# Kernel tuning notes

Measured on AMD Instinct MI355X. Metric: run time of the kernel, lower is better.

The kernel has to match this reference:

```python
import jax, jax.numpy as jnp
from jax import lax
import numpy as np


def setup_inputs() -> dict:
    key = jax.random.key(0)
    ks = jax.random.split(key, 10)
    B, C, T, H, W = 4, 128, 32, 24, 24
    M, k_t, k_s, mix_k = 3, 3, 3, 3
    s = 0.05
    q = jax.random.normal(ks[0], (B, C, T, H, W), jnp.float32)
    k = jax.random.normal(ks[1], (B, C, T, H, W), jnp.float32)
    v = jax.random.normal(ks[2], (B, C, T, H, W), jnp.float32)
    # depthwise 3D kernel banks: [M, C, 1, k_t, k_s, k_s] (OIDHW per branch, groups=C)
    Wk = jax.random.normal(ks[3], (M, C, 1, k_t, k_s, k_s), jnp.float32) * s
    Wv = jax.random.normal(ks[4], (M, C, 1, k_t, k_s, k_s), jnp.float32) * s
    # mix predictor: 1x1 conv1d (pointwise) + causal conv1d C->M
    pre_w = jax.random.normal(ks[5], (C, C), jnp.float32) * s
    pre_b = jax.random.normal(ks[6], (C,), jnp.float32) * s
    mix_w = jax.random.normal(ks[7], (M, C, mix_k), jnp.float32) * s
    mix_b = jax.random.normal(ks[8], (M,), jnp.float32) * s
    return {"q": q, "k": k, "v": v, "Wk": Wk, "Wv": Wv,
            "pre_w": pre_w, "pre_b": pre_b, "mix_w": mix_w, "mix_b": mix_b}


def _mix_alpha(q, pre_w, pre_b, mix_w, mix_b):
    # q: [B,C,T,H,W] -> global spatial pool -> [B,C,T]
    qg = q.mean(axis=(3, 4))
    h = jnp.einsum('oc,bct->bot', pre_w, qg) + pre_b[None, :, None]
    h = jax.nn.gelu(h, approximate=False)  # torch nn.GELU default = exact
    mix_k = mix_w.shape[-1]
    logits = lax.conv_general_dilated(
        h, mix_w, window_strides=(1,), padding=[(mix_k - 1, 0)],
        dimension_numbers=('NCH', 'OIH', 'NCH')) + mix_b[None, :, None]
    return jax.nn.softmax(logits, axis=1)  # [B,M,T]


def _dwconv3d_causal(x, w):
    # x: [B,C,T,H,W], w: [C,1,k_t,k_h,k_w] depthwise (groups=C)
    C = x.shape[1]
    k_t, k_h, k_w = w.shape[2], w.shape[3], w.shape[4]
    pad = [(k_t - 1, 0), (k_h // 2, k_h // 2), (k_w // 2, k_w // 2)]
    return lax.conv_general_dilated(
        x, w, window_strides=(1, 1, 1), padding=pad,
        dimension_numbers=('NCDHW', 'OIDHW', 'NCDHW'),
        feature_group_count=C)


def reference(q, k, v, Wk, Wv, pre_w, pre_b, mix_w, mix_b):
    alpha = _mix_alpha(q, pre_w, pre_b, mix_w, mix_b)  # [B,M,T]
    # all M depthwise branches at once: [M,B,C,T,H,W]
    km = jax.vmap(_dwconv3d_causal, in_axes=(None, 0))(k, Wk)
    vm = jax.vmap(_dwconv3d_causal, in_axes=(None, 0))(v, Wv)
    # per-time mixture-weighted sum over M
    k_out = jnp.einsum('mbcthw,bmt->bcthw', km, alpha)
    v_out = jnp.einsum('mbcthw,bmt->bcthw', vm, alpha)
    return (k_out, v_out)
```

## Files before the change

### kernel.cpp

```cpp
#include <hip/hip_runtime.h>
#include <math.h>

namespace {
constexpr int Bn = 4, Cn = 128, Tn = 32, Hn = 24, Wn = 24, Mn = 3;
constexpr int HWn = Hn * Wn;
constexpr int TTile = 8;
constexpr int PL = TTile + 2;
constexpr int RS = 28;
constexpr int PSr = 26 * RS;
}

__global__ __launch_bounds__(256) void pool_kernel(const float* __restrict__ q,
                                                   float* __restrict__ qg) {
    int wave = threadIdx.x >> 6;
    int lane = threadIdx.x & 63;
    int plane = blockIdx.x * 4 + wave;
    const float4* p = (const float4*)(q + (size_t)plane * HWn);
    float4 a = p[lane];
    float4 b = p[lane + 64];
    float s = (a.x + a.y) + (a.z + a.w) + (b.x + b.y) + (b.z + b.w);
    if (lane < 16) {
        float4 c = p[128 + lane];
        s += (c.x + c.y) + (c.z + c.w);
    }
#pragma unroll
    for (int off = 32; off > 0; off >>= 1) s += __shfl_down(s, off);
    if (lane == 0) qg[plane] = s * (1.0f / 576.0f);
}

__global__ __launch_bounds__(512) void alpha_kernel(const float* __restrict__ qg,
                                                    const float* __restrict__ pre_w,
                                                    const float* __restrict__ pre_b,
                                                    const float* __restrict__ mix_w,
                                                    const float* __restrict__ mix_b,
                                                    float* __restrict__ alpha) {
    __shared__ float qg_s[Cn * Tn];
    __shared__ float h_s[Cn * (Tn + 2)];
    __shared__ float mw_s[Mn * Cn * 3];
    __shared__ float l_s[Mn * Tn];
    int b = blockIdx.x;
    int tid = threadIdx.x;
    for (int i = tid; i < Cn * Tn / 4; i += 512)
        ((float4*)qg_s)[i] = ((const float4*)(qg + b * Cn * Tn))[i];
    for (int i = tid; i < Mn * Cn * 3; i += 512) mw_s[i] = mix_w[i];
    __syncthreads();
    {
        int o0 = (tid >> 3) * 2;
        int t0 = (tid & 7) * 4;
        float acc0[4] = {0.f, 0.f, 0.f, 0.f};
        float acc1[4] = {0.f, 0.f, 0.f, 0.f};
        const float* w0r = pre_w + (size_t)o0 * Cn;
        const float* w1r = w0r + Cn;
#pragma unroll 4
        for (int cb = 0; cb < Cn; cb += 4) {
            float4 wa = *(const float4*)(w0r + cb);
            float4 wb = *(const float4*)(w1r + cb);
            float w0v[4] = {wa.x, wa.y, wa.z, wa.w};
            float w1v[4] = {wb.x, wb.y, wb.z, wb.w};
            float4 g[4];
#pragma unroll
            for (int j = 0; j < 4; ++j)
                g[j] = *(const float4*)(qg_s + (cb + j) * Tn + t0);
#pragma unroll
            for (int j = 0; j < 4; ++j) {
                acc0[0] += w0v[j] * g[j].x; acc0[1] += w0v[j] * g[j].y;
                acc0[2] += w0v[j] * g[j].z; acc0[3] += w0v[j] * g[j].w;
                acc1[0] += w1v[j] * g[j].x; acc1[1] += w1v[j] * g[j].y;
                acc1[2] += w1v[j] * g[j].z; acc1[3] += w1v[j] * g[j].w;
            }
        }
        float b0 = pre_b[o0], b1 = pre_b[o0 + 1];
        if (t0 == 0) {
            h_s[o0 * (Tn + 2) + 0] = 0.f; h_s[o0 * (Tn + 2) + 1] = 0.f;
            h_s[(o0 + 1) * (Tn + 2) + 0] = 0.f; h_s[(o0 + 1) * (Tn + 2) + 1] = 0.f;
        }
#pragma unroll
        for (int j = 0; j < 4; ++j) {
            float x0 = acc0[j] + b0;
            float x1 = acc1[j] + b1;
            h_s[o0 * (Tn + 2) + 2 + t0 + j] =
                0.5f * x0 * (1.0f + erff(x0 * 0.70710678118654752f));
            h_s[(o0 + 1) * (Tn + 2) + 2 + t0 + j] =
                0.5f * x1 * (1.0f + erff(x1 * 0.70710678118654752f));
        }
    }
    __syncthreads();
    if (tid < Mn * Tn) {
        int m = tid / Tn, t = tid % Tn;
        float acc = mix_b[m];
#pragma unroll 8
        for (int c = 0; c < Cn; ++c) {
            const float* mw = mw_s + (m * Cn + c) * 3;
            const float* hp = h_s + c * (Tn + 2) + t;
            acc += mw[0] * hp[0] + mw[1] * hp[1] + mw[2] * hp[2];
        }
        l_s[m * Tn + t] = acc;
    }
    __syncthreads();
    if (tid < Tn) {
        int t = tid;
        float l0 = l_s[t], l1 = l_s[Tn + t], l2 = l_s[2 * Tn + t];
        float mx = fmaxf(l0, fmaxf(l1, l2));
        float e0 = expf(l0 - mx), e1 = expf(l1 - mx), e2 = expf(l2 - mx);
        float inv = 1.0f / (e0 + e1 + e2);
        alpha[(b * Mn + 0) * Tn + t] = e0 * inv;
        alpha[(b * Mn + 1) * Tn + t] = e1 * inv;
        alpha[(b * Mn + 2) * Tn + t] = e2 * inv;
    }
}

__global__ __launch_bounds__(192) void conv_kernel(const float* __restrict__ kin,
                                                   const float* __restrict__ vin,
                                                   const float* __restrict__ Wk,
                                                   const float* __restrict__ Wv,
                                                   const float* __restrict__ alpha,
                                                   float* __restrict__ out) {
    __shared__ float s[PL * PSr];
    __shared__ float sw[TTile * 27];

    int bid = blockIdx.x;
    int tt = bid & 3;
    int c  = (bid >> 2) & 127;
    int b  = (bid >> 9) & 3;
    int br = bid >> 11;
    int t0 = tt * TTile;
    int tid = threadIdx.x;
    const size_t plane_base = (size_t)(b * Cn + c) * Tn;
    const float* __restrict__ src = br ? vin : kin;
    const float* __restrict__ Wb  = br ? Wv : Wk;

    float4 z4 = make_float4(0.f, 0.f, 0.f, 0.f);
    for (int i = tid; i < PL * PSr / 4; i += 192) ((float4*)s)[i] = z4;
    for (int i = tid; i < TTile * 27; i += 192) {
        int tl = i / 27;
        int widx = i - tl * 27;
        float a0 = alpha[(b * Mn + 0) * Tn + t0 + tl];
        float a1 = alpha[(b * Mn + 1) * Tn + t0 + tl];
        float a2 = alpha[(b * Mn + 2) * Tn + t0 + tl];
        sw[i] = a0 * Wb[(0 * Cn + c) * 27 + widx]
              + a1 * Wb[(1 * Cn + c) * 27 + widx]
              + a2 * Wb[(2 * Cn + c) * 27 + widx];
    }
    __syncthreads();

    for (int idx = tid; idx < PL * 144; idx += 192) {
        int p = idx / 144;
        int cell = idx - p * 144;
        int r = cell / 6;
        int c4 = cell - r * 6;
        int tp = t0 - 2 + p;
        if (tp >= 0) {
            float4 val = *(const float4*)(src + (plane_base + tp) * HWn + r * 24 + c4 * 4);
            float* dst = s + p * PSr + (r + 1) * RS + 1 + c4 * 4;
            dst[0] = val.x; dst[1] = val.y; dst[2] = val.z; dst[3] = val.w;
        }
    }
    __syncthreads();

    int tl = tid / 24;
    int rem = tid - tl * 24;
    int h2 = rem >> 1;
    int wseg = rem & 1;
    int h0 = h2 * 2;
    int w0 = wseg * 12;
    const float* wp = sw + tl * 27;
    float acc0[12], acc1[12];
#pragma unroll
    for (int j = 0; j < 12; ++j) { acc0[j] = 0.f; acc1[j] = 0.f; }
#pragma unroll
    for (int dt = 0; dt < 3; ++dt) {
        const float* w9 = wp + dt * 9;
        const float* pb = s + (tl + dt) * PSr + h0 * RS + w0;
#pragma unroll
        for (int j = 0; j < 4; ++j) {
            const float4* rp = (const float4*)(pb + j * RS);
            float4 f0 = rp[0], f1 = rp[1], f2 = rp[2], f3 = rp[3];
            float f[16] = {f0.x, f0.y, f0.z, f0.w, f1.x, f1.y, f1.z, f1.w,
                           f2.x, f2.y, f2.z, f2.w, f3.x, f3.y, f3.z, f3.w};
            if (j <= 2) {
#pragma unroll
                for (int dw = 0; dw < 3; ++dw) {
                    float wc = w9[j * 3 + dw];
#pragma unroll
                    for (int i = 0; i < 12; ++i) acc0[i] += f[i + dw] * wc;
                }
            }
            if (j >= 1) {
#pragma unroll
                for (int dw = 0; dw < 3; ++dw) {
                    float wc = w9[(j - 1) * 3 + dw];
#pragma unroll
                    for (int i = 0; i < 12; ++i) acc1[i] += f[i + dw] * wc;
                }
            }
        }
    }
    size_t obase = (plane_base + t0 + tl) * HWn + h0 * Wn + w0;
    float* op = out + (br ? (size_t)Bn * Cn * Tn * HWn : 0) + obase;
#pragma unroll
    for (int j = 0; j < 3; ++j) {
        ((float4*)op)[j] = make_float4(acc0[4*j], acc0[4*j+1], acc0[4*j+2], acc0[4*j+3]);
        ((float4*)(op + Wn))[j] = make_float4(acc1[4*j], acc1[4*j+1], acc1[4*j+2], acc1[4*j+3]);
    }
}

extern "C" void kernel_launch(void* const* d_in, const int* in_sizes, int n_in,
                              void* d_out, int out_size, void* d_ws, size_t ws_size,
                              hipStream_t stream) {
    const float* q     = (const float*)d_in[0];
    const float* k     = (const float*)d_in[1];
    const float* v     = (const float*)d_in[2];
    const float* Wk    = (const float*)d_in[3];
    const float* Wv    = (const float*)d_in[4];
    const float* pre_w = (const float*)d_in[5];
    const float* pre_b = (const float*)d_in[6];
    const float* mix_w = (const float*)d_in[7];
    const float* mix_b = (const float*)d_in[8];
    float* out = (float*)d_out;

    float* qg    = (float*)d_ws;
    float* alpha = qg + Bn * Cn * Tn;

    hipLaunchKernelGGL(pool_kernel, dim3(Bn * Cn * Tn / 4), dim3(256), 0, stream, q, qg);
    hipLaunchKernelGGL(alpha_kernel, dim3(Bn), dim3(512), 0, stream,
                       qg, pre_w, pre_b, mix_w, mix_b, alpha);
    hipLaunchKernelGGL(conv_kernel, dim3(2 * Bn * Cn * (Tn / TTile)), dim3(192), 0, stream,
                       k, v, Wk, Wv, alpha, out);
}
```

Baseline: 222.4 us.

## Use unpadded smem rows with register-side halo, double time tile

```diff
diff --git a/kernel.cpp b/kernel.cpp
--- a/kernel.cpp
+++ b/kernel.cpp
@@ -4,10 +4,10 @@
 namespace {
 constexpr int Bn = 4, Cn = 128, Tn = 32, Hn = 24, Wn = 24, Mn = 3;
 constexpr int HWn = Hn * Wn;
-constexpr int TTile = 8;
+constexpr int TTile = 16;
 constexpr int PL = TTile + 2;
-constexpr int RS = 28;
-constexpr int PSr = 26 * RS;
+constexpr int RSf = 24;
+constexpr int PSf = 628;
 }
 
 __global__ __launch_bounds__(256) void pool_kernel(const float* __restrict__ q,
@@ -109,29 +109,38 @@
     }
 }
 
-__global__ __launch_bounds__(192) void conv_kernel(const float* __restrict__ kin,
+__global__ __launch_bounds__(384) void conv_kernel(const float* __restrict__ kin,
                                                    const float* __restrict__ vin,
                                                    const float* __restrict__ Wk,
                                                    const float* __restrict__ Wv,
                                                    const float* __restrict__ alpha,
                                                    float* __restrict__ out) {
-    __shared__ float s[PL * PSr];
+    __shared__ float s[PL * PSf];
     __shared__ float sw[TTile * 27];
 
     int bid = blockIdx.x;
-    int tt = bid & 3;
-    int c  = (bid >> 2) & 127;
-    int b  = (bid >> 9) & 3;
-    int br = bid >> 11;
+    int tt = bid & 1;
+    int c  = (bid >> 1) & 127;
+    int b  = (bid >> 8) & 3;
+    int br = bid >> 10;
     int t0 = tt * TTile;
     int tid = threadIdx.x;
     const size_t plane_base = (size_t)(b * Cn + c) * Tn;
     const float* __restrict__ src = br ? vin : kin;
     const float* __restrict__ Wb  = br ? Wv : Wk;
 
-    float4 z4 = make_float4(0.f, 0.f, 0.f, 0.f);
-    for (int i = tid; i < PL * PSr / 4; i += 192) ((float4*)s)[i] = z4;
-    for (int i = tid; i < TTile * 27; i += 192) {
+    for (int idx = tid; idx < PL * 26 * 6; idx += 384) {
+        int p = idx / 156;
+        int rc = idx - p * 156;
+        int r = rc / 6;
+        int c4 = rc - r * 6;
+        int tp = t0 - 2 + p;
+        float4 val = make_float4(0.f, 0.f, 0.f, 0.f);
+        if (tp >= 0 && r >= 1 && r <= 24)
+            val = *(const float4*)(src + (plane_base + tp) * HWn + (r - 1) * RSf + c4 * 4);
+        *(float4*)(s + p * PSf + r * RSf + c4 * 4) = val;
+    }
+    for (int i = tid; i < TTile * 27; i += 384) {
         int tl = i / 27;
         int widx = i - tl * 27;
         float a0 = alpha[(b * Mn + 0) * Tn + t0 + tl];
@@ -143,40 +152,31 @@
     }
     __syncthreads();
 
-    for (int idx = tid; idx < PL * 144; idx += 192) {
-        int p = idx / 144;
-        int cell = idx - p * 144;
-        int r = cell / 6;
-        int c4 = cell - r * 6;
-        int tp = t0 - 2 + p;
-        if (tp >= 0) {
-            float4 val = *(const float4*)(src + (plane_base + tp) * HWn + r * 24 + c4 * 4);
-            float* dst = s + p * PSr + (r + 1) * RS + 1 + c4 * 4;
-            dst[0] = val.x; dst[1] = val.y; dst[2] = val.z; dst[3] = val.w;
-        }
-    }
-    __syncthreads();
-
     int tl = tid / 24;
     int rem = tid - tl * 24;
     int h2 = rem >> 1;
     int wseg = rem & 1;
     int h0 = h2 * 2;
-    int w0 = wseg * 12;
-    const float* wp = sw + tl * 27;
+    bool w1 = (wseg != 0);
+    const float* wq = sw + tl * 27;
     float acc0[12], acc1[12];
 #pragma unroll
     for (int j = 0; j < 12; ++j) { acc0[j] = 0.f; acc1[j] = 0.f; }
 #pragma unroll
     for (int dt = 0; dt < 3; ++dt) {
-        const float* w9 = wp + dt * 9;
-        const float* pb = s + (tl + dt) * PSr + h0 * RS + w0;
+        const float* w9 = wq + dt * 9;
+        const float* pb = s + (tl + dt) * PSf + h0 * RSf + 8 * wseg;
 #pragma unroll
         for (int j = 0; j < 4; ++j) {
-            const float4* rp = (const float4*)(pb + j * RS);
-            float4 f0 = rp[0], f1 = rp[1], f2 = rp[2], f3 = rp[3];
-            float f[16] = {f0.x, f0.y, f0.z, f0.w, f1.x, f1.y, f1.z, f1.w,
-                           f2.x, f2.y, f2.z, f2.w, f3.x, f3.y, f3.z, f3.w};
+            const float4* rp = (const float4*)(pb + j * RSf);
+            float4 A = rp[0], B = rp[1], C = rp[2], D = rp[3];
+            float cc[16] = {A.x, A.y, A.z, A.w, B.x, B.y, B.z, B.w,
+                            C.x, C.y, C.z, C.w, D.x, D.y, D.z, D.w};
+            float f[14];
+            f[0]  = w1 ? cc[3]  : 0.f;
+#pragma unroll
+            for (int i = 1; i <= 12; ++i) f[i] = w1 ? cc[i + 3] : cc[i - 1];
+            f[13] = w1 ? 0.f    : cc[12];
             if (j <= 2) {
 #pragma unroll
                 for (int dw = 0; dw < 3; ++dw) {
@@ -195,7 +195,7 @@
             }
         }
     }
-    size_t obase = (plane_base + t0 + tl) * HWn + h0 * Wn + w0;
+    size_t obase = (plane_base + t0 + tl) * HWn + h0 * Wn + 12 * wseg;
     float* op = out + (br ? (size_t)Bn * Cn * Tn * HWn : 0) + obase;
 #pragma unroll
     for (int j = 0; j < 3; ++j) {
@@ -224,6 +224,6 @@
     hipLaunchKernelGGL(pool_kernel, dim3(Bn * Cn * Tn / 4), dim3(256), 0, stream, q, qg);
     hipLaunchKernelGGL(alpha_kernel, dim3(Bn), dim3(512), 0, stream,
                        qg, pre_w, pre_b, mix_w, mix_b, alpha);
-    hipLaunchKernelGGL(conv_kernel, dim3(2 * Bn * Cn * (Tn / TTile)), dim3(192), 0, stream,
+    hipLaunchKernelGGL(conv_kernel, dim3(2 * Bn * Cn * (Tn / TTile)), dim3(384), 0, stream,
                        k, v, Wk, Wv, alpha, out);
 }
```

Result: slower. 256.2 us (+15.2%).
